# Optimization experiments

Measured on AMD Instinct MI355X. Metric: run time of the kernel, lower is better.

Reference implementation:

```python
import jax, jax.numpy as jnp
import numpy as np
import math

L, R, B, S, D = 103, 512, 2, 512, 768


def setup_inputs() -> dict:
    key = jax.random.key(0)
    ks = jax.random.split(key, 16)
    n = lambda k, sh, s=1.0: jax.random.normal(k, sh, jnp.float32) * s
    W = 0.02  # weight init scale keeps softmax logits well-conditioned
    return {
        "output": n(ks[0], (B, S, D)),              # BERT sequence output (backbone treated as feature extractor)
        "attention_mask": jnp.ones((B, S), jnp.int32),
        "laws": n(ks[1], (L, R, D)),                # precomputed law representations (laws_rep.pkl)
        "Wq": n(ks[2], (D, D), W), "bq": jnp.zeros((D,), jnp.float32),
        "Wk": n(ks[3], (D, D), W), "bk": jnp.zeros((D,), jnp.float32),
        "Wv": n(ks[4], (D, D), W), "bv": jnp.zeros((D,), jnp.float32),
        "w_law_d": n(ks[5], (D,), W), "b_law_d": jnp.zeros((1,), jnp.float32),
        "w_law1": n(ks[6], (R,), W), "b_law1": jnp.zeros((1,), jnp.float32),
        "w_accu_d": n(ks[7], (D,), W), "b_accu_d": jnp.zeros((1,), jnp.float32),
        "w_accu1": n(ks[8], (R,), W), "b_accu1": jnp.zeros((1,), jnp.float32),
        "W_accu2": n(ks[9], (119, L), W), "b_accu2": jnp.zeros((119,), jnp.float32),
        "w_term_d": n(ks[10], (D,), W), "b_term_d": jnp.zeros((1,), jnp.float32),
        "w_term1": n(ks[11], (R,), W), "b_term1": jnp.zeros((1,), jnp.float32),
        "W_term2": n(ks[12], (11, L), W), "b_term2": jnp.zeros((11,), jnp.float32),
    }


def _forward(output, mask_f, laws, Wq, bq, Wk, bk, Wv, bv,
             w_law_d, b_law_d, w_law1, b_law1,
             w_accu_d, b_accu_d, w_accu1, b_accu1, W_accu2, b_accu2,
             w_term_d, b_term_d, w_term1, b_term1, W_term2, b_term2):
    laws_q = laws @ Wq + bq          # [L,R,D]
    facts_k = output @ Wk + bk       # [B,S,D]
    facts_v = output @ Wv + bv       # [B,S,D]
    # relevance: [L,B,R,S]
    scores = jnp.einsum('lrd,bsd->lbrs', laws_q, facts_k) / math.sqrt(768)
    scores = scores + (1.0 - mask_f)[None, :, None, :] * -10000.0
    probs = jax.nn.softmax(scores, axis=-1)          # (dropout omitted: eval mode)
    a_facts = jnp.einsum('lbrs,bsd->lbrd', probs, facts_v)
    g = jnp.transpose(a_facts, (1, 0, 2, 3))         # [B,L,R,D]
    act = jnp.tanh
    # law head: law1(tanh(law_d(g)))  -> [B,L]
    law = act(jnp.einsum('blrd,d->blr', g, w_law_d) + b_law_d)
    law = jnp.einsum('blr,r->bl', law, w_law1) + b_law1
    # accu head: accu2(tanh(accu1(tanh(accu_d(g))))) -> [B,119]
    accu = act(jnp.einsum('blrd,d->blr', g, w_accu_d) + b_accu_d)
    accu = act(jnp.einsum('blr,r->bl', accu, w_accu1) + b_accu1)
    accu = accu @ W_accu2.T + b_accu2
    # term head -> [B,11]
    term = act(jnp.einsum('blrd,d->blr', g, w_term_d) + b_term_d)
    term = act(jnp.einsum('blr,r->bl', term, w_term1) + b_term1)
    term = term @ W_term2.T + b_term2
    return law, accu, term


def reference(output, attention_mask, laws, Wq, bq, Wk, bk, Wv, bv,
              w_law_d, b_law_d, w_law1, b_law1,
              w_accu_d, b_accu_d, w_accu1, b_accu1, W_accu2, b_accu2,
              w_term_d, b_term_d, w_term1, b_term1, W_term2, b_term2):
    mask_f = attention_mask.astype(jnp.float32)
    return _forward(output, mask_f, laws, Wq, bq, Wk, bk, Wv, bv,
                    w_law_d, b_law_d, w_law1, b_law1,
                    w_accu_d, b_accu_d, w_accu1, b_accu1, W_accu2, b_accu2,
                    w_term_d, b_term_d, w_term1, b_term1, W_term2, b_term2)
```

## Files before the change

kernel.cpp:

```cpp
#include <hip/hip_runtime.h>

static constexpr int nL = 103, nR = 512, nB = 2, nS = 512, nD = 768;
static constexpr float INV_SQRT_D = 0.03608439182435161f;

typedef short bf16x8 __attribute__((ext_vector_type(8)));
typedef float f32x4 __attribute__((ext_vector_type(4)));
typedef unsigned short u16;
typedef unsigned short ushort4v __attribute__((ext_vector_type(4)));
typedef unsigned short ushort8v __attribute__((ext_vector_type(8)));

static constexpr size_t OFF_WQB  = 0;
static constexpr size_t OFF_WKB  = 294912;
static constexpr size_t OFF_KQB  = 0;
static constexpr size_t OFF_OUTB = 589824;
static constexpr size_t OFF_MBF  = 983040;
static constexpr size_t OFF_QBK  = 1277952;
static constexpr size_t OFF_WKBQ = OFF_QBK + 768;
static constexpr size_t OFF_WV3  = OFF_WKBQ + 768;
static constexpr size_t OFF_CST  = OFF_WV3 + 2304;
static constexpr size_t OFF_C    = OFF_CST + 4;
static constexpr size_t OFF_HV   = OFF_C + 1024;
static constexpr size_t OFF_SUM  = OFF_HV + 3072;

__device__ inline float wredsum(float v) {
#pragma unroll
  for (int o = 32; o; o >>= 1) v += __shfl_xor(v, o);
  return v;
}

__device__ inline u16 f2bf(float f) {
  unsigned u = __builtin_bit_cast(unsigned, f);
  u += 0x7FFFu + ((u >> 16) & 1u);
  return (u16)(u >> 16);
}

__global__ __launch_bounds__(256) void k_prep(
    const float* __restrict__ Wq, const float* __restrict__ Wk,
    const float* __restrict__ Wv, const float* __restrict__ bq,
    const float* __restrict__ bk, const float* __restrict__ bv,
    const float* __restrict__ wld, const float* __restrict__ wad,
    const float* __restrict__ wtd, float* __restrict__ ws) {
  int tid = threadIdx.x, lane = tid & 63, w = tid >> 6;
  if (blockIdx.x < 192) {
    int row = blockIdx.x * 4 + w;
    const float* wqr = Wq + (size_t)row * nD;
    const float* wkr = Wk + (size_t)row * nD;
    const float* wvr = Wv + (size_t)row * nD;
    float dq = 0.f, dk = 0.f, d0 = 0.f, d1 = 0.f, d2 = 0.f;
#pragma unroll
    for (int k = 0; k < 3; ++k) {
      int off = lane * 4 + k * 256;
      float4 q4 = *(const float4*)(wqr + off);
      float4 k4 = *(const float4*)(wkr + off);
      float4 v4 = *(const float4*)(wvr + off);
      float4 bk4 = *(const float4*)(bk + off);
      float4 bq4 = *(const float4*)(bq + off);
      float4 l4 = *(const float4*)(wld + off);
      float4 a4 = *(const float4*)(wad + off);
      float4 t4 = *(const float4*)(wtd + off);
      dq += q4.x*bk4.x + q4.y*bk4.y + q4.z*bk4.z + q4.w*bk4.w;
      dk += k4.x*bq4.x + k4.y*bq4.y + k4.z*bq4.z + k4.w*bq4.w;
      d0 += v4.x*l4.x + v4.y*l4.y + v4.z*l4.z + v4.w*l4.w;
      d1 += v4.x*a4.x + v4.y*a4.y + v4.z*a4.z + v4.w*a4.w;
      d2 += v4.x*t4.x + v4.y*t4.y + v4.z*t4.z + v4.w*t4.w;
    }
    dq = wredsum(dq); dk = wredsum(dk);
    d0 = wredsum(d0); d1 = wredsum(d1); d2 = wredsum(d2);
    if (lane == 0) {
      ws[OFF_QBK + row] = dq;
      ws[OFF_WKBQ + row] = dk;
      ws[OFF_WV3 + row] = d0;
      ws[OFF_WV3 + 768 + row] = d1;
      ws[OFF_WV3 + 1536 + row] = d2;
    }
  } else {
    if (tid < 64) {
      float c0 = 0.f, c1 = 0.f, c2 = 0.f, c3 = 0.f;
      for (int j = lane; j < nD; j += 64) {
        c0 += bq[j]*bk[j]; c1 += bv[j]*wld[j]; c2 += bv[j]*wad[j]; c3 += bv[j]*wtd[j];
      }
      c0 = wredsum(c0); c1 = wredsum(c1); c2 = wredsum(c2); c3 = wredsum(c3);
      if (lane == 0) {
        ws[OFF_CST+0] = c0; ws[OFF_CST+1] = c1; ws[OFF_CST+2] = c2; ws[OFF_CST+3] = c3;
      }
    }
    for (int i = tid; i < 3 * nB * nL; i += 256) ws[OFF_SUM + i] = 0.f;
  }
}

__global__ __launch_bounds__(256) void k_pack(const float* __restrict__ Wq,
                                              const float* __restrict__ Wk,
                                              const float* __restrict__ outp,
                                              u16* __restrict__ wqb,
                                              u16* __restrict__ wkb,
                                              u16* __restrict__ outb) {
  int bid = blockIdx.x;
  const float* src; u16* dst; int base;
  if (bid < 144)      { src = Wq;   dst = wqb;  base = bid; }
  else if (bid < 288) { src = Wk;   dst = wkb;  base = bid - 144; }
  else                { src = outp; dst = outb; base = bid - 288; }
  size_t e = ((size_t)base * 256 + threadIdx.x) * 16;
  float4 f0 = *(const float4*)(src + e);
  float4 f1 = *(const float4*)(src + e + 4);
  float4 f2 = *(const float4*)(src + e + 8);
  float4 f3 = *(const float4*)(src + e + 12);
  ushort8v u0, u1;
  u0[0]=f2bf(f0.x); u0[1]=f2bf(f0.y); u0[2]=f2bf(f0.z); u0[3]=f2bf(f0.w);
  u0[4]=f2bf(f1.x); u0[5]=f2bf(f1.y); u0[6]=f2bf(f1.z); u0[7]=f2bf(f1.w);
  u1[0]=f2bf(f2.x); u1[1]=f2bf(f2.y); u1[2]=f2bf(f2.z); u1[3]=f2bf(f2.w);
  u1[4]=f2bf(f3.x); u1[5]=f2bf(f3.y); u1[6]=f2bf(f3.z); u1[7]=f2bf(f3.w);
  *(ushort8v*)(dst + e) = u0;
  *(ushort8v*)(dst + e + 8) = u1;
}

__global__ __launch_bounds__(512) void mm_bf(const u16* __restrict__ A,
                                             const u16* __restrict__ B,
                                             u16* __restrict__ C,
                                             const float* __restrict__ bias,
                                             int mode) {
  __shared__ u16 Ast[128 * 40];
  __shared__ u16 Bst[128 * 40];
  const int tid = threadIdx.x, lane = tid & 63, w = tid >> 6;
  const int c4 = lane & 15, q4 = lane >> 4, wr = w >> 2, wc = w & 3;
  const int m0 = blockIdx.y * 128, n0 = blockIdx.x * 128;
  const int sr = tid >> 2, seg = tid & 3;
  const u16* Asrc = A + (size_t)(m0 + sr) * 768 + seg * 8;
  const u16* Bsrc = B + (size_t)(n0 + sr) * 768 + seg * 8;
  f32x4 acc[4][2];
#pragma unroll
  for (int rt = 0; rt < 4; ++rt)
#pragma unroll
    for (int ct = 0; ct < 2; ++ct) acc[rt][ct] = (f32x4){0.f,0.f,0.f,0.f};
  for (int kt = 0; kt < 24; ++kt) {
    ushort8v av = *(const ushort8v*)(Asrc + kt * 32);
    ushort8v bv = *(const ushort8v*)(Bsrc + kt * 32);
    __syncthreads();
    *(ushort8v*)&Ast[sr * 40 + seg * 8] = av;
    *(ushort8v*)&Bst[sr * 40 + seg * 8] = bv;
    __syncthreads();
    bf16x8 af[4], bf[2];
#pragma unroll
    for (int rt = 0; rt < 4; ++rt)
      af[rt] = *(const bf16x8*)&Ast[(wr * 64 + rt * 16 + c4) * 40 + q4 * 8];
#pragma unroll
    for (int ct = 0; ct < 2; ++ct)
      bf[ct] = *(const bf16x8*)&Bst[(wc * 32 + ct * 16 + c4) * 40 + q4 * 8];
#pragma unroll
    for (int rt = 0; rt < 4; ++rt)
#pragma unroll
      for (int ct = 0; ct < 2; ++ct)
        acc[rt][ct] = __builtin_amdgcn_mfma_f32_16x16x32_bf16(af[rt], bf[ct],
                                                              acc[rt][ct], 0, 0, 0);
  }
#pragma unroll
  for (int rt = 0; rt < 4; ++rt)
#pragma unroll
    for (int ct = 0; ct < 2; ++ct) {
      int n = n0 + wc * 32 + ct * 16 + c4;
      float bb = (mode == 1) ? bias[n] : 0.0f;
#pragma unroll
      for (int reg = 0; reg < 4; ++reg) {
        int m = m0 + wr * 64 + rt * 16 + q4 * 4 + reg;
        float v = acc[rt][ct][reg] + bb;
        if (mode == 0) C[(size_t)m * 768 + n] = f2bf(v);
        else C[(((size_t)(n >> 3)) << 13) + ((size_t)m << 3) + (n & 7)] = f2bf(v);
      }
    }
}

__global__ __launch_bounds__(256) void k_chv(const float* __restrict__ outp,
                                             float* __restrict__ ws) {
  int tid = threadIdx.x, lane = tid & 63, w = tid >> 6;
  int idx = blockIdx.x * 4 + w;
  const float* row = outp + (size_t)idx * nD;
  const float* wkbq = ws + OFF_WKBQ;
  const float* wv0 = ws + OFF_WV3;
  const float* wv1 = ws + OFF_WV3 + 768;
  const float* wv2 = ws + OFF_WV3 + 1536;
  float a0 = 0.f, a1 = 0.f, a2 = 0.f, a3 = 0.f;
#pragma unroll
  for (int k = 0; k < 3; ++k) {
    int off = lane * 4 + k * 256;
    float4 o4 = *(const float4*)(row + off);
    float4 k4 = *(const float4*)(wkbq + off);
    float4 l4 = *(const float4*)(wv0 + off);
    float4 c4 = *(const float4*)(wv1 + off);
    float4 t4 = *(const float4*)(wv2 + off);
    a0 += o4.x*k4.x + o4.y*k4.y + o4.z*k4.z + o4.w*k4.w;
    a1 += o4.x*l4.x + o4.y*l4.y + o4.z*l4.z + o4.w*l4.w;
    a2 += o4.x*c4.x + o4.y*c4.y + o4.z*c4.z + o4.w*c4.w;
    a3 += o4.x*t4.x + o4.y*t4.y + o4.z*t4.z + o4.w*t4.w;
  }
  a0 = wredsum(a0); a1 = wredsum(a1); a2 = wredsum(a2); a3 = wredsum(a3);
  if (lane == 0) {
    ws[OFF_C + idx]         = a0 + ws[OFF_CST+0];
    ws[OFF_HV + idx]        = a1 + ws[OFF_CST+1];
    ws[OFF_HV + 1024 + idx] = a2 + ws[OFF_CST+2];
    ws[OFF_HV + 2048 + idx] = a3 + ws[OFF_CST+3];
  }
}

__global__ __launch_bounds__(1024, 4) void k_attn(
    const float* __restrict__ laws, const u16* __restrict__ kqB,
    const int* __restrict__ mask, float* __restrict__ ws,
    const float* __restrict__ bld, const float* __restrict__ wl1,
    const float* __restrict__ bad, const float* __restrict__ wa1,
    const float* __restrict__ btd, const float* __restrict__ wt1) {
  __shared__ u16 Abuf[2][5120];
  __shared__ f32x4 redS[8][128];
  const int tid = threadIdx.x, lane = tid & 63, w = tid >> 6;
  const int c4 = lane & 15, q4 = lane >> 4, wr = w >> 3, wc = w & 7;
  const int b = blockIdx.x, rtile = blockIdx.y, l = blockIdx.z;

  const int sr = tid >> 3, sq = tid & 7;
  const float* Asrc = laws + ((size_t)l * nR + rtile * 128 + sr) * nD + sq * 4;
  u16* Aw = &Abuf[0][sr * 40 + sq * 4];

  {
    float4 g = *(const float4*)(Asrc);
    ushort4v u;
    u[0]=f2bf(g.x); u[1]=f2bf(g.y); u[2]=f2bf(g.z); u[3]=f2bf(g.w);
    *(ushort4v*)Aw = u;
  }

  const u16* Bbase = kqB + ((size_t)q4 * 1024 + (size_t)b * nS + wc * 64 + c4) * 8;

  f32x4 acc[4][4];
#pragma unroll
  for (int rt = 0; rt < 4; ++rt)
#pragma unroll
    for (int ct = 0; ct < 4; ++ct) acc[rt][ct] = (f32x4){0.f,0.f,0.f,0.f};
  __syncthreads();

  for (int kt = 0; kt < 24; ++kt) {
    float4 g; const bool more = kt < 23;
    if (more) g = *(const float4*)(Asrc + (kt + 1) * 32);
    bf16x8 bfr[4];
#pragma unroll
    for (int ct = 0; ct < 4; ++ct)
      bfr[ct] = *(const bf16x8*)(Bbase + ((size_t)kt << 15) + (ct << 7));
    const u16* Ab = &Abuf[kt & 1][0];
    bf16x8 af[4];
#pragma unroll
    for (int rt = 0; rt < 4; ++rt)
      af[rt] = *(const bf16x8*)&Ab[(wr * 64 + rt * 16 + c4) * 40 + q4 * 8];
#pragma unroll
    for (int rt = 0; rt < 4; ++rt)
#pragma unroll
      for (int ct = 0; ct < 4; ++ct)
        acc[rt][ct] = __builtin_amdgcn_mfma_f32_16x16x32_bf16(af[rt], bfr[ct],
                                                              acc[rt][ct], 0, 0, 0);
    if (more) {
      ushort4v u;
      u[0]=f2bf(g.x); u[1]=f2bf(g.y); u[2]=f2bf(g.z); u[3]=f2bf(g.w);
      *(ushort4v*)(Aw + ((kt + 1) & 1) * 5120) = u;
    }
    __syncthreads();
  }

  const float* cp  = ws + OFF_C + (size_t)b * nS;
  const float* hlp = ws + OFF_HV + (size_t)b * nS;
  const float* hap = ws + OFF_HV + 1024 + (size_t)b * nS;
  const float* htp = ws + OFF_HV + 2048 + (size_t)b * nS;
  float cc[4], hl[4], ha[4], ht[4], ma[4];
#pragma unroll
  for (int ct = 0; ct < 4; ++ct) {
    int s = wc * 64 + ct * 16 + c4;
    cc[ct] = cp[s]; hl[ct] = hlp[s]; ha[ct] = hap[s]; ht[ct] = htp[s];
    ma[ct] = (1.0f - (float)mask[b * nS + s]) * -10000.0f;
  }

#pragma unroll
  for (int rt = 0; rt < 4; ++rt) {
#pragma unroll
    for (int reg = 0; reg < 4; ++reg) {
      float sse = 0.f, spl = 0.f, spa = 0.f, spt = 0.f;
#pragma unroll
      for (int ct = 0; ct < 4; ++ct) {
        float x = (acc[rt][ct][reg] + cc[ct]) * INV_SQRT_D + ma[ct];
        float e = __expf(x);
        sse += e; spl += e * hl[ct]; spa += e * ha[ct]; spt += e * ht[ct];
      }
#pragma unroll
      for (int o = 1; o < 16; o <<= 1) {
        sse += __shfl_xor(sse, o);
        spl += __shfl_xor(spl, o);
        spa += __shfl_xor(spa, o);
        spt += __shfl_xor(spt, o);
      }
      if (c4 == 0)
        redS[wc][wr * 64 + rt * 16 + q4 * 4 + reg] = (f32x4){sse, spl, spa, spt};
    }
  }
  __syncthreads();

  if (w < 2) {
    int row = w * 64 + lane;
    f32x4 t = (f32x4){0.f,0.f,0.f,0.f};
#pragma unroll
    for (int wci = 0; wci < 8; ++wci) t += redS[wci][row];
    float inv = 1.0f / t[0];
    int r = rtile * 128 + row;
    float cl = tanhf(t[1] * inv + bld[0]) * wl1[r];
    float ca = tanhf(t[2] * inv + bad[0]) * wa1[r];
    float ctv = tanhf(t[3] * inv + btd[0]) * wt1[r];
#pragma unroll
    for (int o = 1; o < 64; o <<= 1) {
      cl += __shfl_xor(cl, o);
      ca += __shfl_xor(ca, o);
      ctv += __shfl_xor(ctv, o);
    }
    if (lane == 0) {
      float* sums = ws + OFF_SUM;
      atomicAdd(&sums[b * nL + l], cl);
      atomicAdd(&sums[nB * nL + b * nL + l], ca);
      atomicAdd(&sums[2 * nB * nL + b * nL + l], ctv);
    }
  }
}

__global__ void k_final(const float* __restrict__ ws, float* __restrict__ out,
                        const float* __restrict__ bl1, const float* __restrict__ ba1,
                        const float* __restrict__ Wa2, const float* __restrict__ ba2,
                        const float* __restrict__ bt1, const float* __restrict__ Wt2,
                        const float* __restrict__ bt2) {
  __shared__ float abl[nB * nL], tbl[nB * nL];
  int t = threadIdx.x;
  const float* sl = ws + OFF_SUM;
  const float* sa = sl + nB * nL;
  const float* st = sa + nB * nL;
  if (t < nB * nL) {
    out[t] = sl[t] + bl1[0];
    abl[t] = tanhf(sa[t] + ba1[0]);
    tbl[t] = tanhf(st[t] + bt1[0]);
  }
  __syncthreads();
  for (int idx = t; idx < nB * 119; idx += 256) {
    int b = idx / 119, j = idx % 119;
    float a = ba2[j];
    for (int ll = 0; ll < nL; ++ll) a += Wa2[j * nL + ll] * abl[b * nL + ll];
    out[nB * nL + idx] = a;
  }
  for (int idx = t; idx < nB * 11; idx += 256) {
    int b = idx / 11, j = idx % 11;
    float a = bt2[j];
    for (int ll = 0; ll < nL; ++ll) a += Wt2[j * nL + ll] * tbl[b * nL + ll];
    out[nB * nL + nB * 119 + idx] = a;
  }
}

extern "C" void kernel_launch(void* const* d_in, const int* in_sizes, int n_in,
                              void* d_out, int out_size, void* d_ws, size_t ws_size,
                              hipStream_t stream) {
  (void)in_sizes; (void)n_in; (void)out_size; (void)ws_size;
  const float* outp = (const float*)d_in[0];
  const int*   mask = (const int*)d_in[1];
  const float* laws = (const float*)d_in[2];
  const float* Wq = (const float*)d_in[3];  const float* bq = (const float*)d_in[4];
  const float* Wk = (const float*)d_in[5];  const float* bk = (const float*)d_in[6];
  const float* Wv = (const float*)d_in[7];  const float* bv = (const float*)d_in[8];
  const float* wld = (const float*)d_in[9];  const float* bld = (const float*)d_in[10];
  const float* wl1 = (const float*)d_in[11]; const float* bl1 = (const float*)d_in[12];
  const float* wad = (const float*)d_in[13]; const float* bad = (const float*)d_in[14];
  const float* wa1 = (const float*)d_in[15]; const float* ba1 = (const float*)d_in[16];
  const float* Wa2 = (const float*)d_in[17]; const float* ba2 = (const float*)d_in[18];
  const float* wtd = (const float*)d_in[19]; const float* btd = (const float*)d_in[20];
  const float* wt1 = (const float*)d_in[21]; const float* bt1 = (const float*)d_in[22];
  const float* Wt2 = (const float*)d_in[23]; const float* bt2 = (const float*)d_in[24];
  float* ws = (float*)d_ws;
  float* fout = (float*)d_out;
  u16* wqb  = (u16*)(ws + OFF_WQB);
  u16* wkb  = (u16*)(ws + OFF_WKB);
  u16* outb = (u16*)(ws + OFF_OUTB);
  u16* Mbf  = (u16*)(ws + OFF_MBF);
  u16* kqB  = (u16*)(ws + OFF_KQB);

  k_prep<<<193, 256, 0, stream>>>(Wq, Wk, Wv, bq, bk, bv, wld, wad, wtd, ws);
  k_pack<<<480, 256, 0, stream>>>(Wq, Wk, outp, wqb, wkb, outb);
  mm_bf<<<dim3(6, 6), 512, 0, stream>>>(wqb, wkb, Mbf, nullptr, 0);
  mm_bf<<<dim3(6, 8), 512, 0, stream>>>(outb, Mbf, kqB, ws + OFF_QBK, 1);
  k_chv<<<256, 256, 0, stream>>>(outp, ws);
  k_attn<<<dim3(nB, 4, nL), 1024, 0, stream>>>(laws, kqB, mask, ws,
                                               bld, wl1, bad, wa1, btd, wt1);
  k_final<<<1, 256, 0, stream>>>(ws, fout, bl1, ba1, Wa2, ba2, bt1, Wt2, bt2);
}
```

Before: 513.8 us.

## Fuse prep kernels, drop LDS staging in small GEMMs, retile attention with register prefetch

Merges the bf16 packing of the sequence output into the prep kernel. The Wq·Wkᵀ GEMM now converts fp32 on the fly and shares a launch with the per-token projection kernel, and the second GEMM becomes a direct-global-load kernel on smaller 64x64 tiles. The attention kernel moves from 1024-thread blocks with 128 law rows to 512-thread blocks with 64 rows, and adds register double-buffering of the K fragments and a two-step-ahead prefetch of laws. The aim is fewer launches, fewer intermediate buffers, better occupancy and less load latency in the dominant attention GEMM. In exchange, each block reloads shared K fragments more often and register pressure rises.

```diff
diff --git a/kernel.cpp b/kernel.cpp
--- a/kernel.cpp
+++ b/kernel.cpp
@@ -9,12 +9,10 @@
 typedef unsigned short ushort4v __attribute__((ext_vector_type(4)));
 typedef unsigned short ushort8v __attribute__((ext_vector_type(8)));
 
-static constexpr size_t OFF_WQB  = 0;
-static constexpr size_t OFF_WKB  = 294912;
-static constexpr size_t OFF_KQB  = 0;
-static constexpr size_t OFF_OUTB = 589824;
-static constexpr size_t OFF_MBF  = 983040;
-static constexpr size_t OFF_QBK  = 1277952;
+static constexpr size_t OFF_OUTB = 0;
+static constexpr size_t OFF_MBF  = 393216;
+static constexpr size_t OFF_KQB  = 688128;
+static constexpr size_t OFF_QBK  = 1081344;
 static constexpr size_t OFF_WKBQ = OFF_QBK + 768;
 static constexpr size_t OFF_WV3  = OFF_WKBQ + 768;
 static constexpr size_t OFF_CST  = OFF_WV3 + 2304;
@@ -34,15 +32,24 @@
   return (u16)(u >> 16);
 }
 
+__device__ inline bf16x8 cvt8(float4 a, float4 b) {
+  ushort8v u;
+  u[0]=f2bf(a.x); u[1]=f2bf(a.y); u[2]=f2bf(a.z); u[3]=f2bf(a.w);
+  u[4]=f2bf(b.x); u[5]=f2bf(b.y); u[6]=f2bf(b.z); u[7]=f2bf(b.w);
+  return __builtin_bit_cast(bf16x8, u);
+}
+
 __global__ __launch_bounds__(256) void k_prep(
     const float* __restrict__ Wq, const float* __restrict__ Wk,
     const float* __restrict__ Wv, const float* __restrict__ bq,
     const float* __restrict__ bk, const float* __restrict__ bv,
     const float* __restrict__ wld, const float* __restrict__ wad,
-    const float* __restrict__ wtd, float* __restrict__ ws) {
+    const float* __restrict__ wtd, const float* __restrict__ outp,
+    float* __restrict__ ws) {
   int tid = threadIdx.x, lane = tid & 63, w = tid >> 6;
-  if (blockIdx.x < 192) {
-    int row = blockIdx.x * 4 + w;
+  int bid = blockIdx.x;
+  if (bid < 192) {
+    int row = bid * 4 + w;
     const float* wqr = Wq + (size_t)row * nD;
     const float* wkr = Wk + (size_t)row * nD;
     const float* wvr = Wv + (size_t)row * nD;
@@ -73,7 +80,7 @@
       ws[OFF_WV3 + 768 + row] = d1;
       ws[OFF_WV3 + 1536 + row] = d2;
     }
-  } else {
+  } else if (bid == 192) {
     if (tid < 64) {
       float c0 = 0.f, c1 = 0.f, c2 = 0.f, c3 = 0.f;
       for (int j = lane; j < nD; j += 64) {
@@ -85,146 +92,170 @@
       }
     }
     for (int i = tid; i < 3 * nB * nL; i += 256) ws[OFF_SUM + i] = 0.f;
-  }
-}
-
-__global__ __launch_bounds__(256) void k_pack(const float* __restrict__ Wq,
-                                              const float* __restrict__ Wk,
-                                              const float* __restrict__ outp,
-                                              u16* __restrict__ wqb,
-                                              u16* __restrict__ wkb,
-                                              u16* __restrict__ outb) {
+  } else {
+    u16* outb = (u16*)(ws + OFF_OUTB);
+    size_t e = ((size_t)(bid - 193) * 256 + tid) * 16;
+    float4 f0 = *(const float4*)(outp + e);
+    float4 f1 = *(const float4*)(outp + e + 4);
+    float4 f2 = *(const float4*)(outp + e + 8);
+    float4 f3 = *(const float4*)(outp + e + 12);
+    *(ushort8v*)(outb + e)     = __builtin_bit_cast(ushort8v, cvt8(f0, f1));
+    *(ushort8v*)(outb + e + 8) = __builtin_bit_cast(ushort8v, cvt8(f2, f3));
+  }
+}
+
+__global__ __launch_bounds__(256) void k_mmM_chv(
+    const float* __restrict__ Wq, const float* __restrict__ Wk,
+    const float* __restrict__ outp, float* __restrict__ ws) {
+  int tid = threadIdx.x, lane = tid & 63, w = tid >> 6;
   int bid = blockIdx.x;
-  const float* src; u16* dst; int base;
-  if (bid < 144)      { src = Wq;   dst = wqb;  base = bid; }
-  else if (bid < 288) { src = Wk;   dst = wkb;  base = bid - 144; }
-  else                { src = outp; dst = outb; base = bid - 288; }
-  size_t e = ((size_t)base * 256 + threadIdx.x) * 16;
-  float4 f0 = *(const float4*)(src + e);
-  float4 f1 = *(const float4*)(src + e + 4);
-  float4 f2 = *(const float4*)(src + e + 8);
-  float4 f3 = *(const float4*)(src + e + 12);
-  ushort8v u0, u1;
-  u0[0]=f2bf(f0.x); u0[1]=f2bf(f0.y); u0[2]=f2bf(f0.z); u0[3]=f2bf(f0.w);
-  u0[4]=f2bf(f1.x); u0[5]=f2bf(f1.y); u0[6]=f2bf(f1.z); u0[7]=f2bf(f1.w);
-  u1[0]=f2bf(f2.x); u1[1]=f2bf(f2.y); u1[2]=f2bf(f2.z); u1[3]=f2bf(f2.w);
-  u1[4]=f2bf(f3.x); u1[5]=f2bf(f3.y); u1[6]=f2bf(f3.z); u1[7]=f2bf(f3.w);
-  *(ushort8v*)(dst + e) = u0;
-  *(ushort8v*)(dst + e + 8) = u1;
-}
-
-__global__ __launch_bounds__(512) void mm_bf(const u16* __restrict__ A,
-                                             const u16* __restrict__ B,
-                                             u16* __restrict__ C,
-                                             const float* __restrict__ bias,
-                                             int mode) {
-  __shared__ u16 Ast[128 * 40];
-  __shared__ u16 Bst[128 * 40];
-  const int tid = threadIdx.x, lane = tid & 63, w = tid >> 6;
-  const int c4 = lane & 15, q4 = lane >> 4, wr = w >> 2, wc = w & 3;
-  const int m0 = blockIdx.y * 128, n0 = blockIdx.x * 128;
-  const int sr = tid >> 2, seg = tid & 3;
-  const u16* Asrc = A + (size_t)(m0 + sr) * 768 + seg * 8;
-  const u16* Bsrc = B + (size_t)(n0 + sr) * 768 + seg * 8;
-  f32x4 acc[4][2];
-#pragma unroll
-  for (int rt = 0; rt < 4; ++rt)
-#pragma unroll
-    for (int ct = 0; ct < 2; ++ct) acc[rt][ct] = (f32x4){0.f,0.f,0.f,0.f};
+  if (bid < 144) {
+    u16* Mbf = (u16*)(ws + OFF_MBF);
+    const int ti = bid / 12, tj = bid % 12;
+    const int c4 = lane & 15, q4 = lane >> 4, wr = w >> 1, wc = w & 1;
+    f32x4 acc[2][2];
+#pragma unroll
+    for (int i = 0; i < 2; ++i)
+#pragma unroll
+      for (int j = 0; j < 2; ++j) acc[i][j] = (f32x4){0.f,0.f,0.f,0.f};
+    const float* Ab[2]; const float* Bb[2];
+#pragma unroll
+    for (int i = 0; i < 2; ++i)
+      Ab[i] = Wq + (size_t)(ti*64 + wr*32 + i*16 + c4) * nD + q4*8;
+#pragma unroll
+    for (int j = 0; j < 2; ++j)
+      Bb[j] = Wk + (size_t)(tj*64 + wc*32 + j*16 + c4) * nD + q4*8;
+    for (int kt = 0; kt < 24; ++kt) {
+      bf16x8 af[2], bf[2];
+#pragma unroll
+      for (int i = 0; i < 2; ++i)
+        af[i] = cvt8(*(const float4*)(Ab[i] + kt*32), *(const float4*)(Ab[i] + kt*32 + 4));
+#pragma unroll
+      for (int j = 0; j < 2; ++j)
+        bf[j] = cvt8(*(const float4*)(Bb[j] + kt*32), *(const float4*)(Bb[j] + kt*32 + 4));
+#pragma unroll
+      for (int i = 0; i < 2; ++i)
+#pragma unroll
+        for (int j = 0; j < 2; ++j)
+          acc[i][j] = __builtin_amdgcn_mfma_f32_16x16x32_bf16(af[i], bf[j], acc[i][j], 0, 0, 0);
+    }
+#pragma unroll
+    for (int i = 0; i < 2; ++i)
+#pragma unroll
+      for (int j = 0; j < 2; ++j) {
+        int n = tj*64 + wc*32 + j*16 + c4;
+#pragma unroll
+        for (int reg = 0; reg < 4; ++reg) {
+          int m = ti*64 + wr*32 + i*16 + q4*4 + reg;
+          Mbf[(size_t)m * nD + n] = f2bf(acc[i][j][reg]);
+        }
+      }
+  } else {
+    int idx = (bid - 144) * 4 + w;
+    const float* row = outp + (size_t)idx * nD;
+    const float* wkbq = ws + OFF_WKBQ;
+    const float* wv0 = ws + OFF_WV3;
+    const float* wv1 = ws + OFF_WV3 + 768;
+    const float* wv2 = ws + OFF_WV3 + 1536;
+    float a0 = 0.f, a1 = 0.f, a2 = 0.f, a3 = 0.f;
+#pragma unroll
+    for (int k = 0; k < 3; ++k) {
+      int off = lane * 4 + k * 256;
+      float4 o4 = *(const float4*)(row + off);
+      float4 k4 = *(const float4*)(wkbq + off);
+      float4 l4 = *(const float4*)(wv0 + off);
+      float4 c4v = *(const float4*)(wv1 + off);
+      float4 t4 = *(const float4*)(wv2 + off);
+      a0 += o4.x*k4.x + o4.y*k4.y + o4.z*k4.z + o4.w*k4.w;
+      a1 += o4.x*l4.x + o4.y*l4.y + o4.z*l4.z + o4.w*l4.w;
+      a2 += o4.x*c4v.x + o4.y*c4v.y + o4.z*c4v.z + o4.w*c4v.w;
+      a3 += o4.x*t4.x + o4.y*t4.y + o4.z*t4.z + o4.w*t4.w;
+    }
+    a0 = wredsum(a0); a1 = wredsum(a1); a2 = wredsum(a2); a3 = wredsum(a3);
+    if (lane == 0) {
+      ws[OFF_C + idx]         = a0 + ws[OFF_CST+0];
+      ws[OFF_HV + idx]        = a1 + ws[OFF_CST+1];
+      ws[OFF_HV + 1024 + idx] = a2 + ws[OFF_CST+2];
+      ws[OFF_HV + 2048 + idx] = a3 + ws[OFF_CST+3];
+    }
+  }
+}
+
+__global__ __launch_bounds__(256) void k_mkq(float* __restrict__ ws) {
+  const u16* outb = (const u16*)(ws + OFF_OUTB);
+  const u16* Mbf  = (const u16*)(ws + OFF_MBF);
+  u16* kqB = (u16*)(ws + OFF_KQB);
+  const float* qbk = ws + OFF_QBK;
+  int tid = threadIdx.x, lane = tid & 63, w = tid >> 6;
+  const int c4 = lane & 15, q4 = lane >> 4, wr = w >> 1, wc = w & 1;
+  const int ti = blockIdx.y, tj = blockIdx.x;
+  f32x4 acc[2][2];
+#pragma unroll
+  for (int i = 0; i < 2; ++i)
+#pragma unroll
+    for (int j = 0; j < 2; ++j) acc[i][j] = (f32x4){0.f,0.f,0.f,0.f};
+  const u16* Ab[2]; const u16* Bb[2];
+#pragma unroll
+  for (int i = 0; i < 2; ++i)
+    Ab[i] = outb + (size_t)(ti*64 + wr*32 + i*16 + c4) * nD + q4*8;
+#pragma unroll
+  for (int j = 0; j < 2; ++j)
+    Bb[j] = Mbf + (size_t)(tj*64 + wc*32 + j*16 + c4) * nD + q4*8;
   for (int kt = 0; kt < 24; ++kt) {
-    ushort8v av = *(const ushort8v*)(Asrc + kt * 32);
-    ushort8v bv = *(const ushort8v*)(Bsrc + kt * 32);
-    __syncthreads();
-    *(ushort8v*)&Ast[sr * 40 + seg * 8] = av;
-    *(ushort8v*)&Bst[sr * 40 + seg * 8] = bv;
-    __syncthreads();
-    bf16x8 af[4], bf[2];
-#pragma unroll
-    for (int rt = 0; rt < 4; ++rt)
-      af[rt] = *(const bf16x8*)&Ast[(wr * 64 + rt * 16 + c4) * 40 + q4 * 8];
-#pragma unroll
-    for (int ct = 0; ct < 2; ++ct)
-      bf[ct] = *(const bf16x8*)&Bst[(wc * 32 + ct * 16 + c4) * 40 + q4 * 8];
-#pragma unroll
-    for (int rt = 0; rt < 4; ++rt)
-#pragma unroll
-      for (int ct = 0; ct < 2; ++ct)
-        acc[rt][ct] = __builtin_amdgcn_mfma_f32_16x16x32_bf16(af[rt], bf[ct],
-                                                              acc[rt][ct], 0, 0, 0);
-  }
-#pragma unroll
-  for (int rt = 0; rt < 4; ++rt)
-#pragma unroll
-    for (int ct = 0; ct < 2; ++ct) {
-      int n = n0 + wc * 32 + ct * 16 + c4;
-      float bb = (mode == 1) ? bias[n] : 0.0f;
+    bf16x8 af[2], bf[2];
+#pragma unroll
+    for (int i = 0; i < 2; ++i) af[i] = *(const bf16x8*)(Ab[i] + kt*32);
+#pragma unroll
+    for (int j = 0; j < 2; ++j) bf[j] = *(const bf16x8*)(Bb[j] + kt*32);
+#pragma unroll
+    for (int i = 0; i < 2; ++i)
+#pragma unroll
+      for (int j = 0; j < 2; ++j)
+        acc[i][j] = __builtin_amdgcn_mfma_f32_16x16x32_bf16(af[i], bf[j], acc[i][j], 0, 0, 0);
+  }
+#pragma unroll
+  for (int i = 0; i < 2; ++i)
+#pragma unroll
+    for (int j = 0; j < 2; ++j) {
+      int n = tj*64 + wc*32 + j*16 + c4;
+      float bb = qbk[n];
 #pragma unroll
       for (int reg = 0; reg < 4; ++reg) {
-        int m = m0 + wr * 64 + rt * 16 + q4 * 4 + reg;
-        float v = acc[rt][ct][reg] + bb;
-        if (mode == 0) C[(size_t)m * 768 + n] = f2bf(v);
-        else C[(((size_t)(n >> 3)) << 13) + ((size_t)m << 3) + (n & 7)] = f2bf(v);
-      }
-    }
-}
-
-__global__ __launch_bounds__(256) void k_chv(const float* __restrict__ outp,
-                                             float* __restrict__ ws) {
-  int tid = threadIdx.x, lane = tid & 63, w = tid >> 6;
-  int idx = blockIdx.x * 4 + w;
-  const float* row = outp + (size_t)idx * nD;
-  const float* wkbq = ws + OFF_WKBQ;
-  const float* wv0 = ws + OFF_WV3;
-  const float* wv1 = ws + OFF_WV3 + 768;
-  const float* wv2 = ws + OFF_WV3 + 1536;
-  float a0 = 0.f, a1 = 0.f, a2 = 0.f, a3 = 0.f;
-#pragma unroll
-  for (int k = 0; k < 3; ++k) {
-    int off = lane * 4 + k * 256;
-    float4 o4 = *(const float4*)(row + off);
-    float4 k4 = *(const float4*)(wkbq + off);
-    float4 l4 = *(const float4*)(wv0 + off);
-    float4 c4 = *(const float4*)(wv1 + off);
-    float4 t4 = *(const float4*)(wv2 + off);
-    a0 += o4.x*k4.x + o4.y*k4.y + o4.z*k4.z + o4.w*k4.w;
-    a1 += o4.x*l4.x + o4.y*l4.y + o4.z*l4.z + o4.w*l4.w;
-    a2 += o4.x*c4.x + o4.y*c4.y + o4.z*c4.z + o4.w*c4.w;
-    a3 += o4.x*t4.x + o4.y*t4.y + o4.z*t4.z + o4.w*t4.w;
-  }
-  a0 = wredsum(a0); a1 = wredsum(a1); a2 = wredsum(a2); a3 = wredsum(a3);
-  if (lane == 0) {
-    ws[OFF_C + idx]         = a0 + ws[OFF_CST+0];
-    ws[OFF_HV + idx]        = a1 + ws[OFF_CST+1];
-    ws[OFF_HV + 1024 + idx] = a2 + ws[OFF_CST+2];
-    ws[OFF_HV + 2048 + idx] = a3 + ws[OFF_CST+3];
-  }
-}
-
-__global__ __launch_bounds__(1024, 4) void k_attn(
+        int m = ti*64 + wr*32 + i*16 + q4*4 + reg;
+        kqB[(((size_t)(n >> 3)) << 13) + ((size_t)m << 3) + (n & 7)] =
+            f2bf(acc[i][j][reg] + bb);
+      }
+    }
+}
+
+__global__ __launch_bounds__(512) void k_attn(
     const float* __restrict__ laws, const u16* __restrict__ kqB,
     const int* __restrict__ mask, float* __restrict__ ws,
     const float* __restrict__ bld, const float* __restrict__ wl1,
     const float* __restrict__ bad, const float* __restrict__ wa1,
     const float* __restrict__ btd, const float* __restrict__ wt1) {
-  __shared__ u16 Abuf[2][5120];
-  __shared__ f32x4 redS[8][128];
+  __shared__ u16 Abuf[2][64 * 40];
+  __shared__ f32x4 redS[8][64];
   const int tid = threadIdx.x, lane = tid & 63, w = tid >> 6;
-  const int c4 = lane & 15, q4 = lane >> 4, wr = w >> 3, wc = w & 7;
-  const int b = blockIdx.x, rtile = blockIdx.y, l = blockIdx.z;
+  const int c4 = lane & 15, q4 = lane >> 4;
+  const int b = blockIdx.x, rt8 = blockIdx.y, l = blockIdx.z;
 
   const int sr = tid >> 3, sq = tid & 7;
-  const float* Asrc = laws + ((size_t)l * nR + rtile * 128 + sr) * nD + sq * 4;
+  const float* Asrc = laws + ((size_t)l * nR + rt8 * 64 + sr) * nD + sq * 4;
   u16* Aw = &Abuf[0][sr * 40 + sq * 4];
 
+  const u16* Bbase = kqB + ((size_t)q4 * 1024 + (size_t)b * nS + w * 64 + c4) * 8;
+
+  float4 g0 = *(const float4*)(Asrc);
+  bf16x8 Bc[4];
+#pragma unroll
+  for (int ct = 0; ct < 4; ++ct) Bc[ct] = *(const bf16x8*)(Bbase + ct * 128);
+  float4 g1 = *(const float4*)(Asrc + 32);
   {
-    float4 g = *(const float4*)(Asrc);
     ushort4v u;
-    u[0]=f2bf(g.x); u[1]=f2bf(g.y); u[2]=f2bf(g.z); u[3]=f2bf(g.w);
+    u[0]=f2bf(g0.x); u[1]=f2bf(g0.y); u[2]=f2bf(g0.z); u[3]=f2bf(g0.w);
     *(ushort4v*)Aw = u;
   }
-
-  const u16* Bbase = kqB + ((size_t)q4 * 1024 + (size_t)b * nS + wc * 64 + c4) * 8;
-
   f32x4 acc[4][4];
 #pragma unroll
   for (int rt = 0; rt < 4; ++rt)
@@ -232,28 +263,35 @@
     for (int ct = 0; ct < 4; ++ct) acc[rt][ct] = (f32x4){0.f,0.f,0.f,0.f};
   __syncthreads();
 
+#pragma unroll
   for (int kt = 0; kt < 24; ++kt) {
-    float4 g; const bool more = kt < 23;
-    if (more) g = *(const float4*)(Asrc + (kt + 1) * 32);
-    bf16x8 bfr[4];
-#pragma unroll
-    for (int ct = 0; ct < 4; ++ct)
-      bfr[ct] = *(const bf16x8*)(Bbase + ((size_t)kt << 15) + (ct << 7));
+    bf16x8 Bn[4];
+    float4 g2;
+    if (kt < 23) {
+#pragma unroll
+      for (int ct = 0; ct < 4; ++ct)
+        Bn[ct] = *(const bf16x8*)(Bbase + (size_t)(kt + 1) * 32768 + ct * 128);
+    }
+    if (kt < 22)
+      g2 = *(const float4*)(Asrc + (size_t)(kt + 2) * 32);
     const u16* Ab = &Abuf[kt & 1][0];
     bf16x8 af[4];
 #pragma unroll
     for (int rt = 0; rt < 4; ++rt)
-      af[rt] = *(const bf16x8*)&Ab[(wr * 64 + rt * 16 + c4) * 40 + q4 * 8];
+      af[rt] = *(const bf16x8*)&Ab[(rt * 16 + c4) * 40 + q4 * 8];
 #pragma unroll
     for (int rt = 0; rt < 4; ++rt)
 #pragma unroll
       for (int ct = 0; ct < 4; ++ct)
-        acc[rt][ct] = __builtin_amdgcn_mfma_f32_16x16x32_bf16(af[rt], bfr[ct],
+        acc[rt][ct] = __builtin_amdgcn_mfma_f32_16x16x32_bf16(af[rt], Bc[ct],
                                                               acc[rt][ct], 0, 0, 0);
-    if (more) {
+    if (kt < 23) {
       ushort4v u;
-      u[0]=f2bf(g.x); u[1]=f2bf(g.y); u[2]=f2bf(g.z); u[3]=f2bf(g.w);
-      *(ushort4v*)(Aw + ((kt + 1) & 1) * 5120) = u;
+      u[0]=f2bf(g1.x); u[1]=f2bf(g1.y); u[2]=f2bf(g1.z); u[3]=f2bf(g1.w);
+      *(ushort4v*)(Aw + ((kt + 1) & 1) * (64 * 40)) = u;
+      g1 = g2;
+#pragma unroll
+      for (int ct = 0; ct < 4; ++ct) Bc[ct] = Bn[ct];
     }
     __syncthreads();
   }
@@ -265,7 +303,7 @@
   float cc[4], hl[4], ha[4], ht[4], ma[4];
 #pragma unroll
   for (int ct = 0; ct < 4; ++ct) {
-    int s = wc * 64 + ct * 16 + c4;
+    int s = w * 64 + ct * 16 + c4;
     cc[ct] = cp[s]; hl[ct] = hlp[s]; ha[ct] = hap[s]; ht[ct] = htp[s];
     ma[ct] = (1.0f - (float)mask[b * nS + s]) * -10000.0f;
   }
@@ -289,18 +327,18 @@
         spt += __shfl_xor(spt, o);
       }
       if (c4 == 0)
-        redS[wc][wr * 64 + rt * 16 + q4 * 4 + reg] = (f32x4){sse, spl, spa, spt};
+        redS[w][rt * 16 + q4 * 4 + reg] = (f32x4){sse, spl, spa, spt};
     }
   }
   __syncthreads();
 
-  if (w < 2) {
-    int row = w * 64 + lane;
+  if (w == 0) {
+    int row = lane;
     f32x4 t = (f32x4){0.f,0.f,0.f,0.f};
 #pragma unroll
-    for (int wci = 0; wci < 8; ++wci) t += redS[wci][row];
+    for (int wc = 0; wc < 8; ++wc) t += redS[wc][row];
     float inv = 1.0f / t[0];
-    int r = rtile * 128 + row;
+    int r = rt8 * 64 + row;
     float cl = tanhf(t[1] * inv + bld[0]) * wl1[r];
     float ca = tanhf(t[2] * inv + bad[0]) * wa1[r];
     float ctv = tanhf(t[3] * inv + btd[0]) * wt1[r];
@@ -369,18 +407,12 @@
   const float* Wt2 = (const float*)d_in[23]; const float* bt2 = (const float*)d_in[24];
   float* ws = (float*)d_ws;
   float* fout = (float*)d_out;
-  u16* wqb  = (u16*)(ws + OFF_WQB);
-  u16* wkb  = (u16*)(ws + OFF_WKB);
-  u16* outb = (u16*)(ws + OFF_OUTB);
-  u16* Mbf  = (u16*)(ws + OFF_MBF);
-  u16* kqB  = (u16*)(ws + OFF_KQB);
-
-  k_prep<<<193, 256, 0, stream>>>(Wq, Wk, Wv, bq, bk, bv, wld, wad, wtd, ws);
-  k_pack<<<480, 256, 0, stream>>>(Wq, Wk, outp, wqb, wkb, outb);
-  mm_bf<<<dim3(6, 6), 512, 0, stream>>>(wqb, wkb, Mbf, nullptr, 0);
-  mm_bf<<<dim3(6, 8), 512, 0, stream>>>(outb, Mbf, kqB, ws + OFF_QBK, 1);
-  k_chv<<<256, 256, 0, stream>>>(outp, ws);
-  k_attn<<<dim3(nB, 4, nL), 1024, 0, stream>>>(laws, kqB, mask, ws,
-                                               bld, wl1, bad, wa1, btd, wt1);
+  u16* kqB = (u16*)(ws + OFF_KQB);
+
+  k_prep<<<385, 256, 0, stream>>>(Wq, Wk, Wv, bq, bk, bv, wld, wad, wtd, outp, ws);
+  k_mmM_chv<<<400, 256, 0, stream>>>(Wq, Wk, outp, ws);
+  k_mkq<<<dim3(12, 16), 256, 0, stream>>>(ws);
+  k_attn<<<dim3(nB, 8, nL), 512, 0, stream>>>(laws, kqB, mask, ws,
+                                              bld, wl1, bad, wa1, btd, wt1);
   k_final<<<1, 256, 0, stream>>>(ws, fout, bl1, ba1, Wa2, ba2, bt1, Wt2, bt2);
 }
```

Result: faster. 460.2 us (-10.4%).
